# Performance work log

Measured on AMD Instinct MI355X. Metric: run time of the kernel, lower is better.

Reference implementation:

```python
import jax, jax.numpy as jnp
import numpy as np

PHM_DIM = 4
IN_FEATS = 2048
OUT_FEATS = 8192
TOKENS = 8192


def setup_inputs() -> dict:
    key = jax.random.key(0)
    k_x, k_rule, k_w = jax.random.split(key, 3)
    x = jax.random.normal(k_x, (TOKENS, IN_FEATS), dtype=jnp.float32)
    # c_init='normal', std=0.01
    phm_rule = 0.01 * jax.random.normal(k_rule, (PHM_DIM, PHM_DIM, PHM_DIM), dtype=jnp.float32)
    # w_init='normal', std=phm_init_range=1e-4 (scaled up here for numerics of the test)
    W = 1e-4 * jax.random.normal(k_w, (PHM_DIM, IN_FEATS // PHM_DIM, OUT_FEATS // PHM_DIM), dtype=jnp.float32)
    b = jnp.zeros((OUT_FEATS,), dtype=jnp.float32)
    return {"x": x, "phm_rule": phm_rule, "W": W, "b": b}


def reference(x, phm_rule, W, b):
    # H = sum_i kron(phm_rule[i], W[i])  with shape (phm_dim*in_per, phm_dim*out_per)
    # kron(A, B)[a*in_per + c, k*out_per + p] = A[a, k] * B[c, p]
    d, in_per, out_per = W.shape
    H = jnp.einsum('iak,icp->acKp'.replace('K', 'k'), phm_rule, W)  # (d, in_per, d, out_per)
    H = H.reshape(d * in_per, d * out_per)
    y = x @ H + b
    return y
```

## Files before the change

### kernel.cpp

```cpp
#include <hip/hip_runtime.h>
#include <stdint.h>

#define PHM      4
#define IN_FEATS 2048
#define OUT_FEATS 8192
#define TOKENS   8192
#define IN_PER   512
#define OUT_PER  2048

typedef __attribute__((ext_vector_type(8))) short short8;
typedef __attribute__((ext_vector_type(4))) float f32x4;
typedef __attribute__((ext_vector_type(8))) unsigned short u16x8;

__device__ inline unsigned short f2bf(float f) {
    unsigned int u = __builtin_bit_cast(unsigned int, f);
    u += 0x7fffu + ((u >> 16) & 1u);
    return (unsigned short)(u >> 16);
}

__global__ void cvt_x_kernel(const float* __restrict__ x,
                             unsigned short* __restrict__ xb) {
    int i = blockIdx.x * blockDim.x + threadIdx.x;
    const float4* x4 = (const float4*)x;
    float4 v0 = x4[2 * i];
    float4 v1 = x4[2 * i + 1];
    u16x8 o;
    o[0] = f2bf(v0.x); o[1] = f2bf(v0.y); o[2] = f2bf(v0.z); o[3] = f2bf(v0.w);
    o[4] = f2bf(v1.x); o[5] = f2bf(v1.y); o[6] = f2bf(v1.z); o[7] = f2bf(v1.w);
    *(u16x8*)(xb + 8 * (size_t)i) = o;
}

__global__ void build_ht_kernel(const float* __restrict__ rule,
                                const float* __restrict__ W,
                                unsigned short* __restrict__ Ht)
{
    __shared__ float lds[PHM][32][65];
    const int tid = threadIdx.x;
    const int c0 = blockIdx.x * 32;
    const int p0 = blockIdx.y * 64;

    #pragma unroll
    for (int it = 0; it < 32; ++it) {
        int idx = it * 256 + tid;
        int pp = idx & 63;
        int cc = (idx >> 6) & 31;
        int i  = idx >> 11;
        lds[i][cc][pp] = W[((size_t)(i * IN_PER + c0 + cc)) * OUT_PER + p0 + pp];
    }
    __syncthreads();

    const int pp = tid >> 2;
    const int j0 = (tid & 3) * 8;
    float w[PHM][8];
    #pragma unroll
    for (int i = 0; i < PHM; ++i)
        #pragma unroll
        for (int j = 0; j < 8; ++j)
            w[i][j] = lds[i][j0 + j][pp];

    #pragma unroll
    for (int a = 0; a < PHM; ++a) {
        #pragma unroll
        for (int kq = 0; kq < PHM; ++kq) {
            float r0 = rule[(0 * PHM + a) * PHM + kq];
            float r1 = rule[(1 * PHM + a) * PHM + kq];
            float r2 = rule[(2 * PHM + a) * PHM + kq];
            float r3 = rule[(3 * PHM + a) * PHM + kq];
            u16x8 o;
            #pragma unroll
            for (int j = 0; j < 8; ++j) {
                float v = r0 * w[0][j] + r1 * w[1][j] + r2 * w[2][j] + r3 * w[3][j];
                o[j] = f2bf(v);
            }
            size_t n = (size_t)(kq * OUT_PER + p0 + pp);
            *(u16x8*)(Ht + n * IN_FEATS + a * IN_PER + c0 + j0) = o;
        }
    }
}

#define BM 128
#define BN 128
#define BK 32

__device__ inline void load_lds16(const unsigned short* g, unsigned short* l) {
    __builtin_amdgcn_global_load_lds(
        (const __attribute__((address_space(1))) unsigned int*)g,
        (__attribute__((address_space(3))) unsigned int*)l,
        16, 0, 0);
}

__global__ __launch_bounds__(256) void gemm_bt_kernel(
    const unsigned short* __restrict__ A,
    const unsigned short* __restrict__ B,
    const float* __restrict__ bias,
    float* __restrict__ C)
{
    constexpr int N = OUT_FEATS, K = IN_FEATS;
    __shared__ unsigned short As[BM * BK];
    __shared__ unsigned short Bs[BN * BK];

    const int tid  = threadIdx.x;
    const int wave = tid >> 6;
    const int lane = tid & 63;
    const int bn = blockIdx.x;
    const int bm = blockIdx.y;

    const int wm = (wave >> 1) * 64;
    const int wn = (wave & 1) * 64;

    const int s_row = lane >> 2;
    const int s_col = (lane & 3) * 8;

    const unsigned short* Ag = A + ((size_t)(bm * BM + wave * 32 + s_row)) * K + s_col;
    const unsigned short* Bg = B + ((size_t)(bn * BN + wave * 32 + s_row)) * K + s_col;
    unsigned short* As_w = &As[(wave * 32) * BK];
    unsigned short* Bs_w = &Bs[(wave * 32) * BK];

    const int fm = lane & 15;
    const int fk = (lane >> 4) * 8;

    f32x4 acc[4][4] = {};

    for (int k0 = 0; k0 < K; k0 += BK) {
        __syncthreads();
        load_lds16(Ag + k0,          As_w);
        load_lds16(Ag + 16 * K + k0, As_w + 16 * BK);
        load_lds16(Bg + k0,          Bs_w);
        load_lds16(Bg + 16 * K + k0, Bs_w + 16 * BK);
        __syncthreads();

        short8 af[4], bf[4];
        #pragma unroll
        for (int t = 0; t < 4; ++t)
            af[t] = *(const short8*)&As[(wm + t * 16 + fm) * BK + fk];
        #pragma unroll
        for (int t = 0; t < 4; ++t)
            bf[t] = *(const short8*)&Bs[(wn + t * 16 + fm) * BK + fk];
        #pragma unroll
        for (int i = 0; i < 4; ++i)
            #pragma unroll
            for (int j = 0; j < 4; ++j)
                acc[i][j] = __builtin_amdgcn_mfma_f32_16x16x32_bf16(
                    af[i], bf[j], acc[i][j], 0, 0, 0);
    }

    const int cm = (lane >> 4) * 4;
    const int cn = lane & 15;
    #pragma unroll
    for (int j = 0; j < 4; ++j) {
        int col = bn * BN + wn + j * 16 + cn;
        float bv = bias[col];
        #pragma unroll
        for (int i = 0; i < 4; ++i) {
            int row0 = bm * BM + wm + i * 16 + cm;
            #pragma unroll
            for (int r = 0; r < 4; ++r)
                C[(size_t)(row0 + r) * N + col] = acc[i][j][r] + bv;
        }
    }
}

extern "C" void kernel_launch(void* const* d_in, const int* in_sizes, int n_in,
                              void* d_out, int out_size, void* d_ws, size_t ws_size,
                              hipStream_t stream) {
    const float* x    = (const float*)d_in[0];
    const float* rule = (const float*)d_in[1];
    const float* W    = (const float*)d_in[2];
    const float* b    = (const float*)d_in[3];
    float* y = (float*)d_out;

    unsigned short* xb = (unsigned short*)d_ws;
    unsigned short* Ht = (unsigned short*)((char*)d_ws +
                         (size_t)TOKENS * IN_FEATS * sizeof(unsigned short));

    cvt_x_kernel<<<(TOKENS * IN_FEATS) / 8 / 256, 256, 0, stream>>>(x, xb);
    build_ht_kernel<<<dim3(IN_PER / 32, OUT_PER / 64), 256, 0, stream>>>(rule, W, Ht);
    gemm_bt_kernel<<<dim3(OUT_FEATS / BN, TOKENS / BM), 256, 0, stream>>>(xb, Ht, b, y);
}
```

Measured before the change: 626.9 us.

## Widen GEMM N-tile to 256 and switch to 32x32x16 bf16 MFMA

```diff
diff --git a/kernel.cpp b/kernel.cpp
--- a/kernel.cpp
+++ b/kernel.cpp
@@ -8,9 +8,9 @@
 #define IN_PER   512
 #define OUT_PER  2048
 
-typedef __attribute__((ext_vector_type(8))) short short8;
-typedef __attribute__((ext_vector_type(4))) float f32x4;
-typedef __attribute__((ext_vector_type(8))) unsigned short u16x8;
+typedef __attribute__((ext_vector_type(8)))  short short8;
+typedef __attribute__((ext_vector_type(16))) float f32x16;
+typedef __attribute__((ext_vector_type(8)))  unsigned short u16x8;
 
 __device__ inline unsigned short f2bf(float f) {
     unsigned int u = __builtin_bit_cast(unsigned int, f);
@@ -79,7 +79,7 @@
 }
 
 #define BM 128
-#define BN 128
+#define BN 256
 #define BK 32
 
 __device__ inline void load_lds16(const unsigned short* g, unsigned short* l) {
@@ -89,7 +89,7 @@
         16, 0, 0);
 }
 
-__global__ __launch_bounds__(256) void gemm_bt_kernel(
+__global__ __launch_bounds__(256, 2) void gemm_bt_kernel(
     const unsigned short* __restrict__ A,
     const unsigned short* __restrict__ B,
     const float* __restrict__ bias,
@@ -106,20 +106,22 @@
     const int bm = blockIdx.y;
 
     const int wm = (wave >> 1) * 64;
-    const int wn = (wave & 1) * 64;
+    const int wn = (wave & 1) * 128;
 
     const int s_row = lane >> 2;
     const int s_col = (lane & 3) * 8;
 
     const unsigned short* Ag = A + ((size_t)(bm * BM + wave * 32 + s_row)) * K + s_col;
-    const unsigned short* Bg = B + ((size_t)(bn * BN + wave * 32 + s_row)) * K + s_col;
+    const unsigned short* Bg = B + ((size_t)(bn * BN + wave * 64 + s_row)) * K + s_col;
     unsigned short* As_w = &As[(wave * 32) * BK];
-    unsigned short* Bs_w = &Bs[(wave * 32) * BK];
+    unsigned short* Bs_w = &Bs[(wave * 64) * BK];
 
-    const int fm = lane & 15;
-    const int fk = (lane >> 4) * 8;
+    const int m   = lane & 31;
+    const int cg  = lane >> 5;
+    const int p0o = cg * 8;
+    const int p1o = (2 + cg) * 8;
 
-    f32x4 acc[4][4] = {};
+    f32x16 acc[2][4] = {};
 
     for (int k0 = 0; k0 < K; k0 += BK) {
         __syncthreads();
@@ -127,35 +129,47 @@
         load_lds16(Ag + 16 * K + k0, As_w + 16 * BK);
         load_lds16(Bg + k0,          Bs_w);
         load_lds16(Bg + 16 * K + k0, Bs_w + 16 * BK);
+        load_lds16(Bg + 32 * K + k0, Bs_w + 32 * BK);
+        load_lds16(Bg + 48 * K + k0, Bs_w + 48 * BK);
+        __builtin_amdgcn_s_waitcnt(0);
         __syncthreads();
 
-        short8 af[4], bf[4];
+        short8 a0[2], a1[2], b0[4], b1[4];
         #pragma unroll
-        for (int t = 0; t < 4; ++t)
-            af[t] = *(const short8*)&As[(wm + t * 16 + fm) * BK + fk];
+        for (int i = 0; i < 2; ++i) {
+            a0[i] = *(const short8*)&As[(wm + i * 32 + m) * BK + p0o];
+            a1[i] = *(const short8*)&As[(wm + i * 32 + m) * BK + p1o];
+        }
         #pragma unroll
-        for (int t = 0; t < 4; ++t)
-            bf[t] = *(const short8*)&Bs[(wn + t * 16 + fm) * BK + fk];
+        for (int j = 0; j < 4; ++j) {
+            b0[j] = *(const short8*)&Bs[(wn + j * 32 + m) * BK + p0o];
+            b1[j] = *(const short8*)&Bs[(wn + j * 32 + m) * BK + p1o];
+        }
         #pragma unroll
-        for (int i = 0; i < 4; ++i)
+        for (int i = 0; i < 2; ++i)
             #pragma unroll
-            for (int j = 0; j < 4; ++j)
-                acc[i][j] = __builtin_amdgcn_mfma_f32_16x16x32_bf16(
-                    af[i], bf[j], acc[i][j], 0, 0, 0);
+            for (int j = 0; j < 4; ++j) {
+                acc[i][j] = __builtin_amdgcn_mfma_f32_32x32x16_bf16(
+                    a0[i], b0[j], acc[i][j], 0, 0, 0);
+                acc[i][j] = __builtin_amdgcn_mfma_f32_32x32x16_bf16(
+                    a1[i], b1[j], acc[i][j], 0, 0, 0);
+            }
     }
 
-    const int cm = (lane >> 4) * 4;
-    const int cn = lane & 15;
+    const int cn    = lane & 31;
+    const int rbase = 4 * (lane >> 5);
     #pragma unroll
     for (int j = 0; j < 4; ++j) {
-        int col = bn * BN + wn + j * 16 + cn;
+        int col = bn * BN + wn + j * 32 + cn;
         float bv = bias[col];
         #pragma unroll
-        for (int i = 0; i < 4; ++i) {
-            int row0 = bm * BM + wm + i * 16 + cm;
+        for (int i = 0; i < 2; ++i) {
+            int row0 = bm * BM + wm + i * 32 + rbase;
             #pragma unroll
-            for (int r = 0; r < 4; ++r)
-                C[(size_t)(row0 + r) * N + col] = acc[i][j][r] + bv;
+            for (int reg = 0; reg < 16; ++reg) {
+                int row = row0 + (reg & 3) + 8 * (reg >> 2);
+                C[(size_t)row * N + col] = acc[i][j][reg] + bv;
+            }
         }
     }
 }
```

Measured after the change: 614.0 us. -2.1%, faster.
